# Performance work log

Measured on AMD Instinct MI355X. Metric: run time of the kernel, lower is better.

The kernel has to match this reference:

```python
import jax, jax.numpy as jnp
import numpy as np

N = 50000          # nodes
E = 800000         # directed edges (before self loops)
H = 2              # attention heads
NEG_SLOPE = 0.2    # PyG GATv2 default
EPS = 1e-5         # GraphNorm eps
DIMS = [(3, 64), (64, 64), (64, 64)]


def _gatv2_layer(x, Wl, Wr, att, b, src, dst):
    # x: [N, din]; Wl, Wr: [din, H*C]; att: [H, C]; b: [C]
    n = x.shape[0]
    h, c = att.shape
    xl = (x @ Wl).reshape(n, h, c)   # source-side transform
    xr = (x @ Wr).reshape(n, h, c)   # target-side transform
    # edge-wise GATv2 score: a . leaky_relu(xl[j] + xr[i])
    e = jax.nn.leaky_relu(xl[src] + xr[dst], NEG_SLOPE)      # [E, H, C]
    logit = jnp.einsum('ehc,hc->eh', e, att)                 # [E, H]
    # segment softmax over incoming edges of each target node
    m = jax.ops.segment_max(logit, dst, num_segments=n)      # [N, H]
    a = jnp.exp(logit - m[dst])
    z = jax.ops.segment_sum(a, dst, num_segments=n)
    alpha = a / z[dst]                                       # [E, H]
    out = jax.ops.segment_sum(alpha[:, :, None] * xl[src], dst, num_segments=n)  # [N, H, C]
    return out.mean(axis=1) + b                              # concat=False -> head mean


def _graph_norm(x, w, b, ms):
    # single-graph GraphNorm: x -> w * (x - ms*mean) / sqrt(var + eps) + b
    mu = x.mean(axis=0)
    o = x - ms * mu
    var = (o * o).mean(axis=0)
    return w * o * jax.lax.rsqrt(var + EPS) + b


def setup_inputs() -> dict:
    key = jax.random.key(0)
    ks = jax.random.split(key, 2 + 3 * len(DIMS))
    inp = {
        'x': jax.random.normal(ks[0], (N, 3), dtype=jnp.float32),
        'edge_index': jax.random.randint(ks[1], (2, E), 0, N, dtype=jnp.int32),
    }
    for i, (din, dout) in enumerate(DIMS, start=1):
        k0, k1, k2 = ks[2 + 3 * (i - 1):2 + 3 * i]
        s_in = np.float32(1.0 / np.sqrt(din))
        s_att = np.float32(1.0 / np.sqrt(dout))
        inp[f'Wl{i}'] = jax.random.normal(k0, (din, H * dout), dtype=jnp.float32) * s_in
        inp[f'Wr{i}'] = jax.random.normal(k1, (din, H * dout), dtype=jnp.float32) * s_in
        inp[f'att{i}'] = jax.random.normal(k2, (H, dout), dtype=jnp.float32) * s_att
        inp[f'b{i}'] = jnp.zeros((dout,), dtype=jnp.float32)
        inp[f'gw{i}'] = jnp.ones((dout,), dtype=jnp.float32)
        inp[f'gb{i}'] = jnp.zeros((dout,), dtype=jnp.float32)
        inp[f'gm{i}'] = jnp.ones((dout,), dtype=jnp.float32)
    return inp


def reference(x, edge_index,
              Wl1, Wr1, att1, b1, gw1, gb1, gm1,
              Wl2, Wr2, att2, b2, gw2, gb2, gm2,
              Wl3, Wr3, att3, b3, gw3, gb3, gm3):
    n = x.shape[0]
    loop = jnp.arange(n, dtype=edge_index.dtype)
    src = jnp.concatenate([edge_index[0], loop])  # add_self_loops=True
    dst = jnp.concatenate([edge_index[1], loop])
    layers = [(Wl1, Wr1, att1, b1, gw1, gb1, gm1),
              (Wl2, Wr2, att2, b2, gw2, gb2, gm2),
              (Wl3, Wr3, att3, b3, gw3, gb3, gm3)]
    for Wl, Wr, att, b, gw, gb, gm in layers:
        x = _gatv2_layer(x, Wl, Wr, att, b, src, dst)
        x = jax.nn.relu(_graph_norm(x, gw, gb, gm))
    return x
```

## Files before the change

### kernel.cpp

```cpp
#include <hip/hip_runtime.h>
#include <math.h>

#define NN 50000
#define NE 800000
#define TE (NE + NN)
#define HC 128
#define NEG_SLOPE 0.2f
#define EPSV 1e-5f
#define NBUCK 64
#define GGRID 782
#define WTB 128
#define ZB 52
#define ZERO_N4 18644

typedef __attribute__((ext_vector_type(8))) short bf16x8;
typedef __attribute__((ext_vector_type(4))) float f32x4;
union BfU { uint4 u; bf16x8 b; };

__device__ __forceinline__ unsigned short f2bf(float x) {
    unsigned u = __float_as_uint(x);
    unsigned r = (u + 0x7fff + ((u >> 16) & 1)) >> 16;
    return (unsigned short)r;
}


__global__ __launch_bounds__(256) void count_k(const int* __restrict__ dst,
                                               int* __restrict__ cnt,
                                               int* __restrict__ rank) {
    int e = blockIdx.x * 256 + threadIdx.x;
    if (e >= TE) return;
    int d = (e < NE) ? dst[e] : (e - NE);
    rank[e] = atomicAdd(&cnt[d], 1);
}

__global__ __launch_bounds__(1024) void scan1_k(const int* __restrict__ cnt,
                                                int* __restrict__ excl,
                                                int* __restrict__ aux) {
    __shared__ int wsum[16];
    int tid = threadIdx.x;
    int gid = blockIdx.x * 1024 + tid;
    int lane = tid & 63, wid = tid >> 6;
    int v = (gid < NN) ? cnt[gid] : 0;
    int x = v;
#pragma unroll
    for (int off = 1; off < 64; off <<= 1) {
        int t = __shfl_up(x, off, 64);
        if (lane >= off) x += t;
    }
    if (lane == 63) wsum[wid] = x;
    __syncthreads();
    if (wid == 0 && lane < 16) {
        int y = wsum[lane];
#pragma unroll
        for (int off = 1; off < 16; off <<= 1) {
            int t = __shfl_up(y, off, 64);
            if (lane >= off) y += t;
        }
        wsum[lane] = y;
    }
    __syncthreads();
    int base = (wid > 0) ? wsum[wid - 1] : 0;
    int incl = base + x;
    if (gid < NN) excl[gid] = incl - v;
    if (tid == 1023) aux[blockIdx.x] = incl;
}

__global__ __launch_bounds__(256) void scatter_k(const int* __restrict__ srcp,
                                                 const int* __restrict__ dstp,
                                                 const int* __restrict__ excl,
                                                 const int* __restrict__ aux,
                                                 const int* __restrict__ rank,
                                                 int* __restrict__ row_ptr,
                                                 int* __restrict__ col,
                                                 int nblk) {
    __shared__ int auxs[64];
    if (threadIdx.x < 64) {
        int lane = threadIdx.x;
        int v = (lane < nblk) ? aux[lane] : 0;
        int x = v;
#pragma unroll
        for (int off = 1; off < 64; off <<= 1) {
            int t = __shfl_up(x, off, 64);
            if (lane >= off) x += t;
        }
        auxs[lane] = x - v;
    }
    __syncthreads();
    int e = blockIdx.x * 256 + threadIdx.x;
    if (e >= TE) return;
    if (e <= NN) row_ptr[e] = (e == NN) ? TE : excl[e] + auxs[e >> 10];
    int s, d;
    if (e < NE) { s = srcp[e]; d = dstp[e]; } else { s = e - NE; d = s; }
    col[excl[d] + auxs[d >> 10] + rank[e]] = s << 8;
}

__device__ __forceinline__ void store_xlp(char* xlp, int row, int c0, const float* a) {
    unsigned hsel = (unsigned)c0 >> 6;
    unsigned dd = (unsigned)c0 & 31;
    unsigned sub = (c0 & 32) ? 2u : 0u;
    char* q = xlp + (size_t)row * 256 + hsel * 128 + 4 * dd + sub;
#pragma unroll
    for (int j = 0; j < 4; ++j)
        *(unsigned short*)(q + 4 * j) = f2bf(a[j]);
}


__global__ __launch_bounds__(256) void init_k(const float* __restrict__ x,
                                              const float* __restrict__ Wl1,
                                              const float* __restrict__ Wr1,
                                              char* __restrict__ xlp,
                                              float* __restrict__ xr,
                                              const float* __restrict__ Wl2,
                                              const float* __restrict__ Wr2,
                                              const float* __restrict__ Wl3,
                                              const float* __restrict__ Wr3,
                                              unsigned short* __restrict__ wt2,
                                              unsigned short* __restrict__ wt3,
                                              float4* __restrict__ zero4) {
    __shared__ float xs[32][72];
    __shared__ float ws[32][260];
    int b = blockIdx.x;
    int tid = threadIdx.x;

    if (b >= GGRID) {
        if (b < GGRID + WTB) {
            int idx = (b - GGRID) * 256 + tid;
            int l = idx >> 14;
            int rem = idx & 16383;
            int k = rem >> 8;
            int c = rem & 255;
            const float* W = (l == 0) ? (c < 128 ? Wl2 : Wr2) : (c < 128 ? Wl3 : Wr3);
            float v = W[k * 128 + (c & 127)];
            unsigned short* wt = (l == 0) ? wt2 : wt3;
            wt[c * 64 + k] = f2bf(v);
        } else {
            float4 zv; zv.x = zv.y = zv.z = zv.w = 0.f;
            for (int i = (b - GGRID - WTB) * 256 + tid; i < ZERO_N4; i += ZB * 256)
                zero4[i] = zv;
        }
        return;
    }

    int row0 = b * 64;
    int row_t = (tid >> 5) * 8;
    int c0 = (tid & 31) * 4;
    const int K = 3;

    float acc0[8][4];
    float acc1[8][4];
#pragma unroll
    for (int i = 0; i < 8; ++i)
#pragma unroll
        for (int j = 0; j < 4; ++j) { acc0[i][j] = 0.f; acc1[i][j] = 0.f; }

    for (int i = tid; i < 64 * K; i += 256) {
        int r = i / K;
        int k = i - r * K;
        int row = row0 + r;
        xs[k][r] = (row < NN) ? x[(size_t)row * K + k] : 0.f;
    }
    for (int i = tid; i < K * 64; i += 256) {
        int k = i >> 6;
        int cq = i & 63;
        const float* srcp = (cq < 32) ? &Wl1[(size_t)k * 128 + cq * 4]
                                      : &Wr1[(size_t)k * 128 + (cq - 32) * 4];
        float4 v = *(const float4*)srcp;
        *(float4*)&ws[k][cq * 4] = v;
    }
    __syncthreads();
    for (int k = 0; k < K; ++k) {
        float4 a0 = *(float4*)&xs[k][row_t];
        float4 a1 = *(float4*)&xs[k][row_t + 4];
        float4 b0 = *(float4*)&ws[k][c0];
        float4 b1 = *(float4*)&ws[k][c0 + 128];
        float av[8] = {a0.x, a0.y, a0.z, a0.w, a1.x, a1.y, a1.z, a1.w};
        float bl[4] = {b0.x, b0.y, b0.z, b0.w};
        float br[4] = {b1.x, b1.y, b1.z, b1.w};
#pragma unroll
        for (int i = 0; i < 8; ++i)
#pragma unroll
            for (int j = 0; j < 4; ++j) {
                acc0[i][j] += av[i] * bl[j];
                acc1[i][j] += av[i] * br[j];
            }
    }
#pragma unroll
    for (int i = 0; i < 8; ++i) {
        int row = row0 + row_t + i;
        if (row < NN) {
            store_xlp(xlp, row, c0, acc0[i]);
            float4 o1; o1.x = acc1[i][0]; o1.y = acc1[i][1]; o1.z = acc1[i][2]; o1.w = acc1[i][3];
            *(float4*)&xr[(size_t)row * HC + c0] = o1;
        }
    }
}

__device__ __forceinline__ void reduce_stats(const float* __restrict__ stats,
                                             const float* __restrict__ gw,
                                             const float* __restrict__ gb,
                                             const float* __restrict__ gm,
                                             float (*part)[128],
                                             float* __restrict__ cf_out) {
    int tid = threadIdx.x;
    int w = tid >> 6;
    int lane = tid & 63;
    float s = 0.f, s2 = 0.f;
    for (int b = 16 * w; b < 16 * w + 16; ++b) {
        s += stats[b * 128 + lane];
        s2 += stats[b * 128 + 64 + lane];
    }
    part[w][lane] = s;
    part[w][64 + lane] = s2;
    __syncthreads();
    if (tid < 64) {
        int c = tid;
        float sum = (part[0][c] + part[1][c]) + (part[2][c] + part[3][c]);
        float sum2 = (part[0][64 + c] + part[1][64 + c]) + (part[2][64 + c] + part[3][64 + c]);
        float inv_n = 1.f / (float)NN;
        float mu = sum * inv_n;
        float ex2 = sum2 * inv_n;
        float g = gm[c];
        float var = ex2 - 2.f * g * mu * mu + g * g * mu * mu;
        float rs = rsqrtf(var + EPSV);
        cf_out[c] = gw[c] * rs;
        cf_out[64 + c] = gb[c] - gw[c] * rs * g * mu;
    }
    __syncthreads();
}


__global__ __launch_bounds__(256) void gemm_mfma(const unsigned* __restrict__ hbf,
                                                 const float* __restrict__ stats,
                                                 const float* __restrict__ gw,
                                                 const float* __restrict__ gb,
                                                 const float* __restrict__ gm,
                                                 const unsigned short* __restrict__ wt,
                                                 char* __restrict__ xlp,
                                                 float* __restrict__ xr,
                                                 int n) {
    __shared__ unsigned short xs[64][72];
    __shared__ float part[4][128];
    __shared__ float cfS[128];
    int tid = threadIdx.x;
    int row0 = blockIdx.x * 64;

    reduce_stats(stats, gw, gb, gm, part, cfS);

    {
        int r = tid >> 2;
        int q = tid & 3;
        int row = row0 + r;
        unsigned pk[8];
        if (row < n) {
            const unsigned* hp = hbf + (size_t)row * 32 + (q & 1) * 16;
            uint4 u0 = *(const uint4*)(hp + 0);
            uint4 u1 = *(const uint4*)(hp + 4);
            uint4 u2 = *(const uint4*)(hp + 8);
            uint4 u3 = *(const uint4*)(hp + 12);
            unsigned hv[16] = {u0.x, u0.y, u0.z, u0.w, u1.x, u1.y, u1.z, u1.w,
                               u2.x, u2.y, u2.z, u2.w, u3.x, u3.y, u3.z, u3.w};
            bool hi = (q >> 1) != 0;
#pragma unroll
            for (int i = 0; i < 4; ++i) {
                float4 v;
                v.x = hi ? __uint_as_float(hv[4 * i + 0] & 0xffff0000u) : __uint_as_float(hv[4 * i + 0] << 16);
                v.y = hi ? __uint_as_float(hv[4 * i + 1] & 0xffff0000u) : __uint_as_float(hv[4 * i + 1] << 16);
                v.z = hi ? __uint_as_float(hv[4 * i + 2] & 0xffff0000u) : __uint_as_float(hv[4 * i + 2] << 16);
                v.w = hi ? __uint_as_float(hv[4 * i + 3] & 0xffff0000u) : __uint_as_float(hv[4 * i + 3] << 16);
                float4 cw = *(const float4*)&cfS[q * 16 + 4 * i];
                float4 cb = *(const float4*)&cfS[64 + q * 16 + 4 * i];
                float r0 = fmaxf(fmaf(cw.x, v.x, cb.x), 0.f);
                float r1 = fmaxf(fmaf(cw.y, v.y, cb.y), 0.f);
                float r2 = fmaxf(fmaf(cw.z, v.z, cb.z), 0.f);
                float r3 = fmaxf(fmaf(cw.w, v.w, cb.w), 0.f);
                pk[2 * i]     = (unsigned)f2bf(r0) | ((unsigned)f2bf(r1) << 16);
                pk[2 * i + 1] = (unsigned)f2bf(r2) | ((unsigned)f2bf(r3) << 16);
            }
        } else {
#pragma unroll
            for (int i = 0; i < 8; ++i) pk[i] = 0;
        }
        uint4* dst = (uint4*)&xs[r][q * 16];
        dst[0] = make_uint4(pk[0], pk[1], pk[2], pk[3]);
        dst[1] = make_uint4(pk[4], pk[5], pk[6], pk[7]);
    }
    __syncthreads();

    int w = tid >> 6;
    int lane = tid & 63;
    int m = lane & 15;
    int quad = lane >> 4;

    BfU a0, a1;
    a0.u = *(const uint4*)&xs[16 * w + m][quad * 8];
    a1.u = *(const uint4*)&xs[16 * w + m][32 + quad * 8];

    const char* wtb = (const char*)wt + (size_t)(m * 128 + quad * 16);

    f32x4 acc[16];
#pragma unroll
    for (int c = 0; c < 16; ++c) acc[c] = (f32x4){0.f, 0.f, 0.f, 0.f};
#pragma unroll
    for (int c = 0; c < 16; ++c) {
        BfU b0, b1;
        b0.u = *(const uint4*)(wtb + c * 2048);
        b1.u = *(const uint4*)(wtb + c * 2048 + 64);
        acc[c] = __builtin_amdgcn_mfma_f32_16x16x32_bf16(a0.b, b0.b, acc[c], 0, 0, 0);
        acc[c] = __builtin_amdgcn_mfma_f32_16x16x32_bf16(a1.b, b1.b, acc[c], 0, 0, 0);
    }

    int rbase = row0 + 16 * w + quad * 4;
#pragma unroll
    for (int c = 8; c < 16; ++c) {
        int colx = 16 * (c - 8) + m;
#pragma unroll
        for (int r = 0; r < 4; ++r) {
            int row = rbase + r;
            if (row < n) xr[(size_t)row * 128 + colx] = acc[c][r];
        }
    }
#pragma unroll
    for (int pi = 0; pi < 4; ++pi) {
        int c = (pi & 1) + (pi >> 1) * 4;
        int head = pi >> 1;
        int dd = (pi & 1) * 16 + m;
#pragma unroll
        for (int r = 0; r < 4; ++r) {
            int row = rbase + r;
            if (row < n) {
                unsigned val = (unsigned)f2bf(acc[c][r]) | ((unsigned)f2bf(acc[c + 2][r]) << 16);
                *(unsigned*)(xlp + (size_t)row * 256 + head * 128 + 4 * dd) = val;
            }
        }
    }
}


__device__ __forceinline__ void unpack8(uint4 q, float* l) {
    l[0] = __uint_as_float(q.x << 16);
    l[1] = __uint_as_float(q.x & 0xffff0000u);
    l[2] = __uint_as_float(q.y << 16);
    l[3] = __uint_as_float(q.y & 0xffff0000u);
    l[4] = __uint_as_float(q.z << 16);
    l[5] = __uint_as_float(q.z & 0xffff0000u);
    l[6] = __uint_as_float(q.w << 16);
    l[7] = __uint_as_float(q.w & 0xffff0000u);
}

__device__ __forceinline__ float logit_part(const float* l,
                                            float4 xv0, float4 xv1,
                                            float4 a0, float4 a1) {
    float u1 = 0.f, u2 = 0.f, t;
    t = l[0] + xv0.x; u1 = fmaf(a0.x, t, u1); u2 = fmaf(a0.x, fabsf(t), u2);
    t = l[1] + xv1.x; u1 = fmaf(a1.x, t, u1); u2 = fmaf(a1.x, fabsf(t), u2);
    t = l[2] + xv0.y; u1 = fmaf(a0.y, t, u1); u2 = fmaf(a0.y, fabsf(t), u2);
    t = l[3] + xv1.y; u1 = fmaf(a1.y, t, u1); u2 = fmaf(a1.y, fabsf(t), u2);
    t = l[4] + xv0.z; u1 = fmaf(a0.z, t, u1); u2 = fmaf(a0.z, fabsf(t), u2);
    t = l[5] + xv1.z; u1 = fmaf(a1.z, t, u1); u2 = fmaf(a1.z, fabsf(t), u2);
    t = l[6] + xv0.w; u1 = fmaf(a0.w, t, u1); u2 = fmaf(a0.w, fabsf(t), u2);
    t = l[7] + xv1.w; u1 = fmaf(a1.w, t, u1); u2 = fmaf(a1.w, fabsf(t), u2);
    return fmaf(0.6f, u1, 0.4f * u2);
}

__device__ __forceinline__ void attn_pair(const char* __restrict__ xlp, int lp16,
                                          int off0, int off1, bool v0, bool v1,
                                          float4 xv0, float4 xv1,
                                          float4 a0, float4 a1,
                                          float* o, float& zacc) {
    uint4 q0 = *(const uint4*)(xlp + (unsigned)(off0 + lp16));
    uint4 q1 = *(const uint4*)(xlp + (unsigned)(off1 + lp16));
    float l0[8], l1[8];
    unpack8(q0, l0);
    unpack8(q1, l1);
    float w0 = logit_part(l0, xv0, xv1, a0, a1);
    float w1 = logit_part(l1, xv0, xv1, a0, a1);
    w0 += __shfl_xor(w0, 1, 64);
    w1 += __shfl_xor(w1, 1, 64);
    w0 += __shfl_xor(w0, 2, 64);
    w1 += __shfl_xor(w1, 2, 64);
    w0 += __shfl_xor(w0, 4, 64);
    w1 += __shfl_xor(w1, 4, 64);
    float e0 = __expf(w0);
    float e1 = __expf(w1);
    if (!v0) e0 = 0.f;
    if (!v1) e1 = 0.f;
    zacc += e0 + e1;
#pragma unroll
    for (int k = 0; k < 8; ++k) o[k] = fmaf(e0, l0[k], o[k]);
#pragma unroll
    for (int k = 0; k < 8; ++k) o[k] = fmaf(e1, l1[k], o[k]);
}

__global__ __launch_bounds__(256) void attn_k(const char* __restrict__ xlp,
                                              const float* __restrict__ xr,
                                              const float* __restrict__ att,
                                              const float* __restrict__ bias,
                                              const int* __restrict__ row_ptr,
                                              const int* __restrict__ coloff,
                                              unsigned* __restrict__ hout,
                                              float* __restrict__ stats) {
    __shared__ float sb[4][64];
    int tid = threadIdx.x;
    int lane = tid & 63;
    int wv = tid >> 6;
    int node = blockIdx.x * 4 + wv;
    int t16 = lane & 15;
    int slot = (lane >> 4) * 2;
    int head = t16 >> 3;
    int dd = (t16 & 7) * 4;
    int lp16 = t16 * 16;
    int cbase = head * 64 + dd;

    const float* xrow = xr + (size_t)node * 128;
    float4 xv0 = *(const float4*)(xrow + cbase);
    float4 xv1 = *(const float4*)(xrow + cbase + 32);
    float4 a0 = *(const float4*)(att + cbase);
    float4 a1 = *(const float4*)(att + cbase + 32);

    float o[8];
#pragma unroll
    for (int k = 0; k < 8; ++k) o[k] = 0.f;
    float zacc = 0.f;

    int beg = __builtin_amdgcn_readfirstlane(row_ptr[node]);
    int end = __builtin_amdgcn_readfirstlane(row_ptr[node + 1]);

    int idx = beg;
    for (; idx + 8 <= end; idx += 8) {
        int off0 = coloff[idx + slot];
        int off1 = coloff[idx + slot + 1];
        attn_pair(xlp, lp16, off0, off1, true, true, xv0, xv1, a0, a1, o, zacc);
    }
    if (idx < end) {
        int e1 = end - 1;
        int i0 = idx + slot, i1 = idx + slot + 1;
        int off0 = coloff[min(i0, e1)];
        int off1 = coloff[min(i1, e1)];
        attn_pair(xlp, lp16, off0, off1, i0 < end, i1 < end, xv0, xv1, a0, a1, o, zacc);
    }

    float z = zacc + __shfl_xor(zacc, 16, 64);
    z += __shfl_xor(z, 32, 64);
    float zi = 1.0f / z;
    float r[8];
#pragma unroll
    for (int k = 0; k < 8; ++k) {
        float v = o[k] + __shfl_xor(o[k], 16, 64);
        v += __shfl_xor(v, 32, 64);
        v *= zi;
        float p = __shfl_xor(v, 8, 64);
        r[k] = 0.5f * (v + p);
    }
    if (lane < 8) {
        float4 b0 = *(const float4*)(bias + dd);
        float4 b1 = *(const float4*)(bias + dd + 32);
        float rl0 = r[0] + b0.x, rl1 = r[2] + b0.y, rl2 = r[4] + b0.z, rl3 = r[6] + b0.w;
        float rh0 = r[1] + b1.x, rh1 = r[3] + b1.y, rh2 = r[5] + b1.z, rh3 = r[7] + b1.w;
        unsigned pk0 = (unsigned)f2bf(rl0) | ((unsigned)f2bf(rh0) << 16);
        unsigned pk1 = (unsigned)f2bf(rl1) | ((unsigned)f2bf(rh1) << 16);
        unsigned pk2 = (unsigned)f2bf(rl2) | ((unsigned)f2bf(rh2) << 16);
        unsigned pk3 = (unsigned)f2bf(rl3) | ((unsigned)f2bf(rh3) << 16);
        *(uint4*)&hout[(size_t)node * 32 + dd] = make_uint4(pk0, pk1, pk2, pk3);
        *(float4*)&sb[wv][dd] = make_float4(rl0, rl1, rl2, rl3);
        *(float4*)&sb[wv][dd + 32] = make_float4(rh0, rh1, rh2, rh3);
    }
    __syncthreads();
    if (tid < 64) {
        int c = tid;
        float v0 = sb[0][c], v1 = sb[1][c], v2 = sb[2][c], v3 = sb[3][c];
        float s = (v0 + v1) + (v2 + v3);
        float s2 = fmaf(v0, v0, v1 * v1) + fmaf(v2, v2, v3 * v3);
        float* bkt = stats + (size_t)(blockIdx.x & (NBUCK - 1)) * 128;
        atomicAdd(&bkt[c], s);
        atomicAdd(&bkt[64 + c], s2);
    }
}


__global__ __launch_bounds__(256) void apply_k(const unsigned* __restrict__ h,
                                               const float* __restrict__ stats,
                                               const float* __restrict__ gw,
                                               const float* __restrict__ gb,
                                               const float* __restrict__ gm,
                                               float* __restrict__ y) {
    __shared__ float part[4][128];
    __shared__ float cfS[128];
    reduce_stats(stats, gw, gb, gm, part, cfS);

    int i = blockIdx.x * 256 + threadIdx.x;
    if (i >= NN * 8) return;
    int node = i >> 3;
    int j = (i & 7) * 4;
    uint4 u = *(const uint4*)(h + (size_t)node * 32 + j);
    float4 lo, hi;
    lo.x = __uint_as_float(u.x << 16); hi.x = __uint_as_float(u.x & 0xffff0000u);
    lo.y = __uint_as_float(u.y << 16); hi.y = __uint_as_float(u.y & 0xffff0000u);
    lo.z = __uint_as_float(u.z << 16); hi.z = __uint_as_float(u.z & 0xffff0000u);
    lo.w = __uint_as_float(u.w << 16); hi.w = __uint_as_float(u.w & 0xffff0000u);
    float4 cwl = *(const float4*)&cfS[j];
    float4 cbl = *(const float4*)&cfS[64 + j];
    float4 cwh = *(const float4*)&cfS[32 + j];
    float4 cbh = *(const float4*)&cfS[96 + j];
    float4 rl, rh;
    rl.x = fmaxf(fmaf(cwl.x, lo.x, cbl.x), 0.f);
    rl.y = fmaxf(fmaf(cwl.y, lo.y, cbl.y), 0.f);
    rl.z = fmaxf(fmaf(cwl.z, lo.z, cbl.z), 0.f);
    rl.w = fmaxf(fmaf(cwl.w, lo.w, cbl.w), 0.f);
    rh.x = fmaxf(fmaf(cwh.x, hi.x, cbh.x), 0.f);
    rh.y = fmaxf(fmaf(cwh.y, hi.y, cbh.y), 0.f);
    rh.z = fmaxf(fmaf(cwh.z, hi.z, cbh.z), 0.f);
    rh.w = fmaxf(fmaf(cwh.w, hi.w, cbh.w), 0.f);
    *(float4*)&y[(size_t)node * 64 + j] = rl;
    *(float4*)&y[(size_t)node * 64 + 32 + j] = rh;
}


extern "C" void kernel_launch(void* const* d_in, const int* in_sizes, int n_in,
                              void* d_out, int out_size, void* d_ws, size_t ws_size,
                              hipStream_t stream) {
    const float* x0 = (const float*)d_in[0];
    const int* ei = (const int*)d_in[1];
    const int* srcp = ei;
    const int* dstp = ei + NE;

    const float* Wl[3], *Wr[3], *att[3], *bv[3], *gw[3], *gb[3], *gm[3];
    for (int l = 0; l < 3; ++l) {
        int base = 2 + 7 * l;
        Wl[l] = (const float*)d_in[base + 0];
        Wr[l] = (const float*)d_in[base + 1];
        att[l] = (const float*)d_in[base + 2];
        bv[l] = (const float*)d_in[base + 3];
        gw[l] = (const float*)d_in[base + 4];
        gb[l] = (const float*)d_in[base + 5];
        gm[l] = (const float*)d_in[base + 6];
    }

    char* p = (char*)d_ws;
    auto take = [&](size_t bytes) -> void* {
        void* r = (void*)p;
        p += (bytes + 255) & ~(size_t)255;
        return r;
    };
    char* xlp = (char*)take((size_t)NN * 256);
    float* xr = (float*)take((size_t)NN * 128 * 4);
    unsigned* hb = (unsigned*)take((size_t)NN * 32 * 4);
    char* zr = (char*)take(298304);
    float* stats = (float*)zr;
    int* cnt = (int*)(zr + 98304);
    int* excl = (int*)take((size_t)NN * 4);
    int* row_ptr = (int*)take((size_t)(NN + 1) * 4);
    int* rank = (int*)take((size_t)TE * 4);
    int* col = (int*)take((size_t)TE * 4);
    int* aux = (int*)take(64 * 4);
    unsigned short* wt2 = (unsigned short*)take(16384 * 2);
    unsigned short* wt3 = (unsigned short*)take(16384 * 2);

    int nblk = (NN + 1023) / 1024;
    int egrid = (TE + 255) / 256;

    init_k<<<GGRID + WTB + ZB, 256, 0, stream>>>(x0, Wl[0], Wr[0], xlp, xr,
                                                 Wl[1], Wr[1], Wl[2], Wr[2],
                                                 wt2, wt3, (float4*)zr);
    count_k<<<egrid, 256, 0, stream>>>(dstp, cnt, rank);
    scan1_k<<<nblk, 1024, 0, stream>>>(cnt, excl, aux);
    scatter_k<<<egrid, 256, 0, stream>>>(srcp, dstp, excl, aux, rank, row_ptr, col, nblk);

    int ggrid = (NN + 63) / 64;
    int agrid = NN / 4;
    for (int l = 0; l < 3; ++l) {
        if (l > 0)
            gemm_mfma<<<ggrid, 256, 0, stream>>>(hb, stats + (size_t)(l - 1) * NBUCK * 128,
                                                 gw[l - 1], gb[l - 1], gm[l - 1],
                                                 (l == 1) ? wt2 : wt3, xlp, xr, NN);
        attn_k<<<agrid, 256, 0, stream>>>(xlp, xr, att[l], bv[l], row_ptr, col, hb,
                                          stats + (size_t)l * NBUCK * 128);
    }
    apply_k<<<(NN * 8 + 255) / 256, 256, 0, stream>>>(hb, stats + (size_t)2 * NBUCK * 128,
                                                      gw[2], gb[2], gm[2], (float*)d_out);
}
```

Measured before the change: 349.1 us.

## Store target-side features as packed bf16 and gather four edges per attention step

The target-side transform xr is now stored in the same packed bf16 interleaved layout as xlp instead of fp32, in both the first-layer init kernel and the MFMA gemm. This halves its write and read traffic and lets the attention kernel load it with one 16-byte load. The attention kernel's main loop also processes 16 edges per iteration (four gathers per thread), giving more loads in flight. In exchange, the target-side features lose precision to bf16, and register pressure rises in the attention loop.

```diff
diff --git a/kernel.cpp b/kernel.cpp
--- a/kernel.cpp
+++ b/kernel.cpp
@@ -109,7 +109,7 @@
                                               const float* __restrict__ Wl1,
                                               const float* __restrict__ Wr1,
                                               char* __restrict__ xlp,
-                                              float* __restrict__ xr,
+                                              char* __restrict__ xrp,
                                               const float* __restrict__ Wl2,
                                               const float* __restrict__ Wr2,
                                               const float* __restrict__ Wl3,
@@ -189,8 +189,7 @@
         int row = row0 + row_t + i;
         if (row < NN) {
             store_xlp(xlp, row, c0, acc0[i]);
-            float4 o1; o1.x = acc1[i][0]; o1.y = acc1[i][1]; o1.z = acc1[i][2]; o1.w = acc1[i][3];
-            *(float4*)&xr[(size_t)row * HC + c0] = o1;
+            store_xlp(xrp, row, c0, acc1[i]);
         }
     }
 }
@@ -236,7 +235,7 @@
                                                  const float* __restrict__ gm,
                                                  const unsigned short* __restrict__ wt,
                                                  char* __restrict__ xlp,
-                                                 float* __restrict__ xr,
+                                                 char* __restrict__ xrp,
                                                  int n) {
     __shared__ unsigned short xs[64][72];
     __shared__ float part[4][128];
@@ -311,15 +310,6 @@
 
     int rbase = row0 + 16 * w + quad * 4;
 #pragma unroll
-    for (int c = 8; c < 16; ++c) {
-        int colx = 16 * (c - 8) + m;
-#pragma unroll
-        for (int r = 0; r < 4; ++r) {
-            int row = rbase + r;
-            if (row < n) xr[(size_t)row * 128 + colx] = acc[c][r];
-        }
-    }
-#pragma unroll
     for (int pi = 0; pi < 4; ++pi) {
         int c = (pi & 1) + (pi >> 1) * 4;
         int head = pi >> 1;
@@ -328,8 +318,10 @@
         for (int r = 0; r < 4; ++r) {
             int row = rbase + r;
             if (row < n) {
-                unsigned val = (unsigned)f2bf(acc[c][r]) | ((unsigned)f2bf(acc[c + 2][r]) << 16);
-                *(unsigned*)(xlp + (size_t)row * 256 + head * 128 + 4 * dd) = val;
+                unsigned vl = (unsigned)f2bf(acc[c][r]) | ((unsigned)f2bf(acc[c + 2][r]) << 16);
+                unsigned vr = (unsigned)f2bf(acc[c + 8][r]) | ((unsigned)f2bf(acc[c + 10][r]) << 16);
+                *(unsigned*)(xlp + (size_t)row * 256 + head * 128 + 4 * dd) = vl;
+                *(unsigned*)(xrp + (size_t)row * 256 + head * 128 + 4 * dd) = vr;
             }
         }
     }
@@ -347,52 +339,73 @@
     l[7] = __uint_as_float(q.w & 0xffff0000u);
 }
 
-__device__ __forceinline__ float logit_part(const float* l,
-                                            float4 xv0, float4 xv1,
-                                            float4 a0, float4 a1) {
-    float u1 = 0.f, u2 = 0.f, t;
-    t = l[0] + xv0.x; u1 = fmaf(a0.x, t, u1); u2 = fmaf(a0.x, fabsf(t), u2);
-    t = l[1] + xv1.x; u1 = fmaf(a1.x, t, u1); u2 = fmaf(a1.x, fabsf(t), u2);
-    t = l[2] + xv0.y; u1 = fmaf(a0.y, t, u1); u2 = fmaf(a0.y, fabsf(t), u2);
-    t = l[3] + xv1.y; u1 = fmaf(a1.y, t, u1); u2 = fmaf(a1.y, fabsf(t), u2);
-    t = l[4] + xv0.z; u1 = fmaf(a0.z, t, u1); u2 = fmaf(a0.z, fabsf(t), u2);
-    t = l[5] + xv1.z; u1 = fmaf(a1.z, t, u1); u2 = fmaf(a1.z, fabsf(t), u2);
-    t = l[6] + xv0.w; u1 = fmaf(a0.w, t, u1); u2 = fmaf(a0.w, fabsf(t), u2);
-    t = l[7] + xv1.w; u1 = fmaf(a1.w, t, u1); u2 = fmaf(a1.w, fabsf(t), u2);
+__device__ __forceinline__ float logit_part(const float* l, const float* xv, const float* av) {
+    float u1 = 0.f, u2 = 0.f;
+#pragma unroll
+    for (int k = 0; k < 8; ++k) {
+        float t = l[k] + xv[k];
+        u1 = fmaf(av[k], t, u1);
+        u2 = fmaf(av[k], fabsf(t), u2);
+    }
     return fmaf(0.6f, u1, 0.4f * u2);
+}
+
+__device__ __forceinline__ float head_reduce(float w) {
+    w += __shfl_xor(w, 1, 64);
+    w += __shfl_xor(w, 2, 64);
+    w += __shfl_xor(w, 4, 64);
+    return w;
 }
 
 __device__ __forceinline__ void attn_pair(const char* __restrict__ xlp, int lp16,
                                           int off0, int off1, bool v0, bool v1,
-                                          float4 xv0, float4 xv1,
-                                          float4 a0, float4 a1,
+                                          const float* xv, const float* av,
                                           float* o, float& zacc) {
     uint4 q0 = *(const uint4*)(xlp + (unsigned)(off0 + lp16));
     uint4 q1 = *(const uint4*)(xlp + (unsigned)(off1 + lp16));
     float l0[8], l1[8];
     unpack8(q0, l0);
     unpack8(q1, l1);
-    float w0 = logit_part(l0, xv0, xv1, a0, a1);
-    float w1 = logit_part(l1, xv0, xv1, a0, a1);
-    w0 += __shfl_xor(w0, 1, 64);
-    w1 += __shfl_xor(w1, 1, 64);
-    w0 += __shfl_xor(w0, 2, 64);
-    w1 += __shfl_xor(w1, 2, 64);
-    w0 += __shfl_xor(w0, 4, 64);
-    w1 += __shfl_xor(w1, 4, 64);
+    float w0 = head_reduce(logit_part(l0, xv, av));
+    float w1 = head_reduce(logit_part(l1, xv, av));
     float e0 = __expf(w0);
     float e1 = __expf(w1);
     if (!v0) e0 = 0.f;
     if (!v1) e1 = 0.f;
     zacc += e0 + e1;
 #pragma unroll
-    for (int k = 0; k < 8; ++k) o[k] = fmaf(e0, l0[k], o[k]);
-#pragma unroll
-    for (int k = 0; k < 8; ++k) o[k] = fmaf(e1, l1[k], o[k]);
+    for (int k = 0; k < 8; ++k) o[k] = fmaf(e1, l1[k], fmaf(e0, l0[k], o[k]));
+}
+
+__device__ __forceinline__ void attn_quad(const char* __restrict__ xlp, int lp16,
+                                          int off0, int off1, int off2, int off3,
+                                          const float* xv, const float* av,
+                                          float* o, float& zacc) {
+    uint4 q0 = *(const uint4*)(xlp + (unsigned)(off0 + lp16));
+    uint4 q1 = *(const uint4*)(xlp + (unsigned)(off1 + lp16));
+    uint4 q2 = *(const uint4*)(xlp + (unsigned)(off2 + lp16));
+    uint4 q3 = *(const uint4*)(xlp + (unsigned)(off3 + lp16));
+    float l0[8], l1[8], l2[8], l3[8];
+    unpack8(q0, l0);
+    unpack8(q1, l1);
+    unpack8(q2, l2);
+    unpack8(q3, l3);
+    float w0 = head_reduce(logit_part(l0, xv, av));
+    float w1 = head_reduce(logit_part(l1, xv, av));
+    float w2 = head_reduce(logit_part(l2, xv, av));
+    float w3 = head_reduce(logit_part(l3, xv, av));
+    float e0 = __expf(w0);
+    float e1 = __expf(w1);
+    float e2 = __expf(w2);
+    float e3 = __expf(w3);
+    zacc += (e0 + e1) + (e2 + e3);
+#pragma unroll
+    for (int k = 0; k < 8; ++k)
+        o[k] = fmaf(e3, l3[k], fmaf(e2, l2[k], fmaf(e1, l1[k], fmaf(e0, l0[k], o[k]))));
 }
 
 __global__ __launch_bounds__(256) void attn_k(const char* __restrict__ xlp,
-                                              const float* __restrict__ xr,
+                                              const char* __restrict__ xrp,
                                               const float* __restrict__ att,
                                               const float* __restrict__ bias,
                                               const int* __restrict__ row_ptr,
@@ -411,11 +424,11 @@
     int lp16 = t16 * 16;
     int cbase = head * 64 + dd;
 
-    const float* xrow = xr + (size_t)node * 128;
-    float4 xv0 = *(const float4*)(xrow + cbase);
-    float4 xv1 = *(const float4*)(xrow + cbase + 32);
+    float xv[8];
+    unpack8(*(const uint4*)(xrp + ((size_t)node << 8) + lp16), xv);
     float4 a0 = *(const float4*)(att + cbase);
     float4 a1 = *(const float4*)(att + cbase + 32);
+    float av[8] = {a0.x, a1.x, a0.y, a1.y, a0.z, a1.z, a0.w, a1.w};
 
     float o[8];
 #pragma unroll
@@ -426,17 +439,25 @@
     int end = __builtin_amdgcn_readfirstlane(row_ptr[node + 1]);
 
     int idx = beg;
-    for (; idx + 8 <= end; idx += 8) {
+    for (; idx + 16 <= end; idx += 16) {
         int off0 = coloff[idx + slot];
         int off1 = coloff[idx + slot + 1];
-        attn_pair(xlp, lp16, off0, off1, true, true, xv0, xv1, a0, a1, o, zacc);
+        int off2 = coloff[idx + 8 + slot];
+        int off3 = coloff[idx + 8 + slot + 1];
+        attn_quad(xlp, lp16, off0, off1, off2, off3, xv, av, o, zacc);
+    }
+    if (idx + 8 <= end) {
+        int off0 = coloff[idx + slot];
+        int off1 = coloff[idx + slot + 1];
+        attn_pair(xlp, lp16, off0, off1, true, true, xv, av, o, zacc);
+        idx += 8;
     }
     if (idx < end) {
         int e1 = end - 1;
         int i0 = idx + slot, i1 = idx + slot + 1;
         int off0 = coloff[min(i0, e1)];
         int off1 = coloff[min(i1, e1)];
-        attn_pair(xlp, lp16, off0, off1, i0 < end, i1 < end, xv0, xv1, a0, a1, o, zacc);
+        attn_pair(xlp, lp16, off0, off1, i0 < end, i1 < end, xv, av, o, zacc);
     }
 
     float z = zacc + __shfl_xor(zacc, 16, 64);
@@ -542,7 +563,7 @@
         return r;
     };
     char* xlp = (char*)take((size_t)NN * 256);
-    float* xr = (float*)take((size_t)NN * 128 * 4);
+    char* xrp = (char*)take((size_t)NN * 256);
     unsigned* hb = (unsigned*)take((size_t)NN * 32 * 4);
     char* zr = (char*)take(298304);
     float* stats = (float*)zr;
@@ -558,7 +579,7 @@
     int nblk = (NN + 1023) / 1024;
     int egrid = (TE + 255) / 256;
 
-    init_k<<<GGRID + WTB + ZB, 256, 0, stream>>>(x0, Wl[0], Wr[0], xlp, xr,
+    init_k<<<GGRID + WTB + ZB, 256, 0, stream>>>(x0, Wl[0], Wr[0], xlp, xrp,
                                                  Wl[1], Wr[1], Wl[2], Wr[2],
                                                  wt2, wt3, (float4*)zr);
     count_k<<<egrid, 256, 0, stream>>>(dstp, cnt, rank);
@@ -571,8 +592,8 @@
         if (l > 0)
             gemm_mfma<<<ggrid, 256, 0, stream>>>(hb, stats + (size_t)(l - 1) * NBUCK * 128,
                                                  gw[l - 1], gb[l - 1], gm[l - 1],
-                                                 (l == 1) ? wt2 : wt3, xlp, xr, NN);
-        attn_k<<<agrid, 256, 0, stream>>>(xlp, xr, att[l], bv[l], row_ptr, col, hb,
+                                                 (l == 1) ? wt2 : wt3, xlp, xrp, NN);
+        attn_k<<<agrid, 256, 0, stream>>>(xlp, xrp, att[l], bv[l], row_ptr, col, hb,
                                           stats + (size_t)l * NBUCK * 128);
     }
     apply_k<<<(NN * 8 + 255) / 256, 256, 0, stream>>>(hb, stats + (size_t)2 * NBUCK * 128,
```

Measured after the change: 358.1 us. 1.03x slower.
